# Optimization experiments

Measured on AMD Instinct MI355X. Metric: run time of the kernel, lower is better.

Reference implementation:

```python
import jax, jax.numpy as jnp
import numpy as np

EPS = 1e-12  # F.normalize eps

def _l2norm(x):
    n = jnp.linalg.norm(x, axis=-1, keepdims=True)
    return x / jnp.maximum(n, EPS)

def setup_inputs() -> dict:
    key = jax.random.key(0)
    ks = jax.random.split(key, 12)
    B, C, D, N, K = 64, 256, 128, 100000, 8
    inp = {
        "query_input": jax.random.normal(ks[0], (B, C), dtype=jnp.float32),
        "keys": jax.random.normal(ks[1], (N, D), dtype=jnp.float32),
        "values": jax.random.normal(ks[2], (N, D), dtype=jnp.float32),
        "importance": jax.random.uniform(ks[3], (N,), dtype=jnp.float32),
        # params (Linear weights stored torch-style: [out, in])
        "W_q": jax.random.normal(ks[4], (D, C), dtype=jnp.float32) / np.sqrt(C),
        "b_q": jax.random.normal(ks[5], (D,), dtype=jnp.float32) * 0.01,
        "w_attn": jax.random.normal(ks[6], (D,), dtype=jnp.float32) / np.sqrt(D),
        "b_attn": jax.random.normal(ks[7], (), dtype=jnp.float32) * 0.01,
        "W_comb": jax.random.normal(ks[8], (D, D), dtype=jnp.float32) / np.sqrt(D),
        "b_comb": jax.random.normal(ks[9], (D,), dtype=jnp.float32) * 0.01,
        "top_k": K,
    }
    return inp

def reference(query_input, keys, values, importance, W_q, b_q, w_attn, b_attn, W_comb, b_comb, top_k):
    # query projection: [B, D]
    q = query_input @ W_q.T + b_q
    # cosine similarity against every bank entry, importance-weighted: [B, N]
    sim = (_l2norm(q) @ _l2norm(keys).T) * importance[None, :]
    # top-k entries per batch row
    _, idx = jax.lax.top_k(sim, top_k)          # [B, K]
    retrieved = values[idx]                      # [B, K, D] gather
    # attention over the K retrieved memories
    scores = jax.nn.softmax(retrieved @ w_attn + b_attn, axis=-1)  # [B, K]
    memory_output = jnp.einsum("bk,bkd->bd", scores, retrieved)
    return memory_output @ W_comb.T + b_comb
```

## Files before the change

kernel.cpp:

```cpp
#include <hip/hip_runtime.h>

typedef __attribute__((ext_vector_type(8))) short short8;
typedef __attribute__((ext_vector_type(4))) float f32x4;

#define BB 64
#define CC 256
#define DD 128
#define NN 100000
#define KK 8

#define CHUNK 128
#define NBLK ((NN + CHUNK - 1) / CHUNK)
#define CPB (NBLK * KK)

__device__ __forceinline__ unsigned short f2bf(float x) {
    unsigned u = __float_as_uint(x);
    unsigned r = u + 0x7fffu + ((u >> 16) & 1u);
    return (unsigned short)(r >> 16);
}

__device__ __forceinline__ void split_bf(float x, unsigned short& h, unsigned short& l) {
    h = f2bf(x);
    float hf = __uint_as_float(((unsigned)h) << 16);
    l = f2bf(x - hf);
}

__device__ __forceinline__ void bfins8(float x, float l[8]) {
#pragma unroll
    for (int s = 0; s < 8; ++s) {
        float hi = fmaxf(l[s], x);
        x = fminf(l[s], x);
        l[s] = hi;
    }
}

__device__ __forceinline__ void bpins8(float v, int ix, float lv[8], int li[8]) {
#pragma unroll
    for (int s = 0; s < 8; ++s) {
        const bool gt = v > lv[s];
        const float nv = gt ? lv[s] : v;
        const int   ni = gt ? li[s] : ix;
        lv[s] = gt ? v : lv[s];
        li[s] = gt ? ix : li[s];
        v = nv; ix = ni;
    }
}

__global__ __launch_bounds__(128) void qproj_kernel(
    const float* __restrict__ query,
    const float* __restrict__ Wq,
    const float* __restrict__ bq,
    unsigned short* __restrict__ qAhi,
    unsigned short* __restrict__ qAlo)
{
    __shared__ float qrow[CC];
    const int tid = threadIdx.x;
    const int b = blockIdx.x;
    for (int i = tid; i < CC; i += 128) qrow[i] = query[b * CC + i];
    __syncthreads();
    float acc = bq[tid];
    const float4* wr = reinterpret_cast<const float4*>(Wq + (size_t)tid * CC);
#pragma unroll 8
    for (int c = 0; c < CC / 4; ++c) {
        float4 w = wr[c];
        acc = fmaf(w.x, qrow[c * 4 + 0], acc);
        acc = fmaf(w.y, qrow[c * 4 + 1], acc);
        acc = fmaf(w.z, qrow[c * 4 + 2], acc);
        acc = fmaf(w.w, qrow[c * 4 + 3], acc);
    }
    unsigned short h, l;
    split_bf(acc, h, l);
    const int d = tid;
    const int mt = b >> 4, n = b & 15;
    const int ks = d >> 5, quad = (d >> 3) & 3, j = d & 7;
    const size_t fi = ((size_t)(mt * 4 + ks) * 64 + quad * 16 + n) * 8 + j;
    qAhi[fi] = h;
    qAlo[fi] = l;
}

__global__ __launch_bounds__(256, 4) void simtopk_kernel(
    const unsigned short* __restrict__ qAhi,
    const unsigned short* __restrict__ qAlo,
    const float* __restrict__ keys,
    const float* __restrict__ imp,
    float* __restrict__ cand_v)
{
    __shared__ float sims[64 * 132];

    const int tid = threadIdx.x;
    const int w = tid >> 6, lane = tid & 63;
    const int p = w >> 1;
    const int h = w & 1;
    const int blk = blockIdx.x;
    const int key0 = blk * CHUNK;
    const int n = lane & 15, quad = lane >> 4;

    short8 Ah[2][4], Al[2][4];
    {
        const short8* GH = reinterpret_cast<const short8*>(qAhi);
        const short8* GL = reinterpret_cast<const short8*>(qAlo);
#pragma unroll
        for (int m2 = 0; m2 < 2; ++m2)
#pragma unroll
            for (int ks = 0; ks < 4; ++ks) {
                const int idx = ((p * 2 + m2) * 4 + ks) * 64 + lane;
                Ah[m2][ks] = GH[idx];
                Al[m2][ks] = GL[idx];
            }
    }

#pragma unroll
    for (int t = 0; t < 4; ++t) {
        const int jl = h * 64 + t * 16 + n;
        const int j = key0 + jl;
        const int jc = (j < NN) ? j : (NN - 1);
        const float* kb = keys + (size_t)jc * DD + quad * 8;

        float4 bv[8];
#pragma unroll
        for (int ks = 0; ks < 4; ++ks) {
            bv[2 * ks]     = *reinterpret_cast<const float4*>(kb + ks * 32);
            bv[2 * ks + 1] = *reinterpret_cast<const float4*>(kb + ks * 32 + 4);
        }

        f32x4 acc[2];
        acc[0] = (f32x4){0.f, 0.f, 0.f, 0.f};
        acc[1] = (f32x4){0.f, 0.f, 0.f, 0.f};
        float ss = 0.f;

#pragma unroll
        for (int ks = 0; ks < 4; ++ks) {
            const float f[8] = {bv[2*ks].x, bv[2*ks].y, bv[2*ks].z, bv[2*ks].w,
                                bv[2*ks+1].x, bv[2*ks+1].y, bv[2*ks+1].z, bv[2*ks+1].w};
            unsigned hw[4], lw[4];
#pragma unroll
            for (int e = 0; e < 4; ++e) {
                const float f0 = f[2 * e], f1 = f[2 * e + 1];
                const unsigned u0 = __float_as_uint(f0), u1 = __float_as_uint(f1);
                hw[e] = __builtin_amdgcn_perm(u1, u0, 0x07060302u);
                const float d0 = f0 - __uint_as_float(u0 & 0xffff0000u);
                const float d1 = f1 - __uint_as_float(u1 & 0xffff0000u);
                lw[e] = __builtin_amdgcn_perm(__float_as_uint(d1), __float_as_uint(d0), 0x07060302u);
                ss = fmaf(f0, f0, fmaf(f1, f1, ss));
            }
            uint4 hv = {hw[0], hw[1], hw[2], hw[3]};
            uint4 lv = {lw[0], lw[1], lw[2], lw[3]};
            short8 Bh = *reinterpret_cast<short8*>(&hv);
            short8 Bl = *reinterpret_cast<short8*>(&lv);
#pragma unroll
            for (int m2 = 0; m2 < 2; ++m2) {
                acc[m2] = __builtin_amdgcn_mfma_f32_16x16x32_bf16(Ah[m2][ks], Bh, acc[m2], 0, 0, 0);
                acc[m2] = __builtin_amdgcn_mfma_f32_16x16x32_bf16(Ah[m2][ks], Bl, acc[m2], 0, 0, 0);
                acc[m2] = __builtin_amdgcn_mfma_f32_16x16x32_bf16(Al[m2][ks], Bh, acc[m2], 0, 0, 0);
            }
        }

        ss += __shfl_xor(ss, 16);
        ss += __shfl_xor(ss, 32);
        const bool valid = (j < NN);
        float scale = 0.f;
        if (valid) scale = imp[j] / fmaxf(sqrtf(ss), 1e-12f);

#pragma unroll
        for (int m2 = 0; m2 < 2; ++m2)
#pragma unroll
            for (int r = 0; r < 4; ++r) {
                const int row = (p * 2 + m2) * 16 + quad * 4 + r;
                const float v = valid ? acc[m2][r] * scale : -1e30f;
                const unsigned packed = (__float_as_uint(v) & ~0x7Fu) | (unsigned)jl;
                sims[row * 132 + jl] = __uint_as_float(packed);
            }
    }
    __syncthreads();

    float v8[8];
    {
        const int row = tid >> 2, part = tid & 3;
#pragma unroll
        for (int s = 0; s < 8; ++s) v8[s] = -1e30f;
        const int base = row * 132 + part * 32;
        const int st = ((row & 15) + part * 8) & 31;
        for (int i = 0; i < 32; ++i) {
            const int ia = (i + st) & 31;
            bfins8(sims[base + ia], v8);
        }
    }
    __syncthreads();

    {
        const int row = tid >> 2, part = tid & 3;
        float4* dst = reinterpret_cast<float4*>(&sims[row * 132 + part * 8]);
        dst[0] = (float4){v8[0], v8[1], v8[2], v8[3]};
        dst[1] = (float4){v8[4], v8[5], v8[6], v8[7]};
    }
    __syncthreads();

    if (tid < 64) {
        const int row = tid;
        float m8[8];
#pragma unroll
        for (int s = 0; s < 8; ++s) m8[s] = -1e30f;
        const int st = (3 * row) & 31;
        for (int u = 0; u < 32; ++u)
            bfins8(sims[row * 132 + ((u + st) & 31)], m8);
        float4* out4 = reinterpret_cast<float4*>(cand_v + (size_t)row * CPB + (size_t)blk * KK);
        out4[0] = (float4){m8[0], m8[1], m8[2], m8[3]};
        out4[1] = (float4){m8[4], m8[5], m8[6], m8[7]};
    }
}

__global__ __launch_bounds__(256) void mergefinish_kernel(
    const float* __restrict__ cand_v,
    const float* __restrict__ values,
    const float* __restrict__ w_attn,
    const float* __restrict__ b_attn,
    const float* __restrict__ W_comb,
    const float* __restrict__ b_comb,
    float* __restrict__ out)
{
    __shared__ float lv[256 * 8];
    __shared__ int   li[256 * 8];
    __shared__ int   tk[KK];
    __shared__ float red[KK][DD];
    __shared__ float tvals[KK];
    __shared__ float mem[DD];

    const int tid = threadIdx.x;
    const int row = blockIdx.x;

    {
        float v8[8]; int i8[8];
#pragma unroll
        for (int s = 0; s < 8; ++s) { v8[s] = -1e30f; i8[s] = 0; }
        const float4* cv4 = reinterpret_cast<const float4*>(cand_v + (size_t)row * CPB);
        for (int c4 = tid; c4 < CPB / 4; c4 += 256) {
            const float4 v = cv4[c4];
            const int c = c4 * 4;
            bpins8(v.x, c + 0, v8, i8);
            bpins8(v.y, c + 1, v8, i8);
            bpins8(v.z, c + 2, v8, i8);
            bpins8(v.w, c + 3, v8, i8);
        }
#pragma unroll
        for (int s = 0; s < 8; ++s) { lv[tid * 8 + s] = v8[s]; li[tid * 8 + s] = i8[s]; }
    }
    __syncthreads();

    if (tid < 64) {
        float m8[8]; int mi8[8];
#pragma unroll
        for (int s = 0; s < 8; ++s) { m8[s] = -1e30f; mi8[s] = 0; }
        for (int k2 = 0; k2 < 4; ++k2)
#pragma unroll
            for (int s = 0; s < 8; ++s)
                bpins8(lv[(tid + 64 * k2) * 8 + s], li[(tid + 64 * k2) * 8 + s], m8, mi8);
        for (int rd = 0; rd < KK; ++rd) {
            float m = m8[0];
#pragma unroll
            for (int d = 1; d < 64; d <<= 1) m = fmaxf(m, __shfl_xor(m, d));
            const unsigned long long msk = __ballot(m8[0] == m);
            const int wl = (int)(__ffsll((long long)msk) - 1);
            const int wc = __shfl(mi8[0], wl);
            if (tid == 0)
                tk[rd] = (wc >> 3) * CHUNK + (int)(__float_as_uint(m) & 127u);
            if (tid == wl) {
#pragma unroll
                for (int s = 0; s < 7; ++s) { m8[s] = m8[s + 1]; mi8[s] = mi8[s + 1]; }
                m8[7] = -1e30f;
            }
        }
    }
    __syncthreads();

    float vk[KK];
    if (tid < 128) {
#pragma unroll
        for (int k = 0; k < KK; ++k)
            vk[k] = values[(size_t)tk[k] * DD + tid];
        const float wa = w_attn[tid];
#pragma unroll
        for (int k = 0; k < KK; ++k) red[k][tid] = vk[k] * wa;
    }
    __syncthreads();
    if (tid < KK) {
        float s = 0.f;
        for (int i = 0; i < DD; ++i) s += red[tid][i];
        tvals[tid] = s + b_attn[0];
    }
    __syncthreads();
    if (tid < 128) {
        float m = tvals[0];
#pragma unroll
        for (int k = 1; k < KK; ++k) m = fmaxf(m, tvals[k]);
        float e[KK]; float se = 0.f;
#pragma unroll
        for (int k = 0; k < KK; ++k) { e[k] = expf(tvals[k] - m); se += e[k]; }
        const float inv = 1.f / se;
        float md = 0.f;
#pragma unroll
        for (int k = 0; k < KK; ++k) md += (e[k] * inv) * vk[k];
        mem[tid] = md;
    }
    __syncthreads();
    if (tid < 128) {
        float acc = b_comb[tid];
        const float4* wrow = reinterpret_cast<const float4*>(W_comb + (size_t)tid * DD);
#pragma unroll 8
        for (int c = 0; c < DD / 4; ++c) {
            float4 wv = wrow[c];
            acc = fmaf(wv.x, mem[c * 4 + 0], acc);
            acc = fmaf(wv.y, mem[c * 4 + 1], acc);
            acc = fmaf(wv.z, mem[c * 4 + 2], acc);
            acc = fmaf(wv.w, mem[c * 4 + 3], acc);
        }
        out[row * DD + tid] = acc;
    }
}

extern "C" void kernel_launch(void* const* d_in, const int* in_sizes, int n_in,
                              void* d_out, int out_size, void* d_ws, size_t ws_size,
                              hipStream_t stream) {
    const float* query  = (const float*)d_in[0];
    const float* keys   = (const float*)d_in[1];
    const float* values = (const float*)d_in[2];
    const float* imp    = (const float*)d_in[3];
    const float* Wq     = (const float*)d_in[4];
    const float* bq     = (const float*)d_in[5];
    const float* wattn  = (const float*)d_in[6];
    const float* battn  = (const float*)d_in[7];
    const float* Wcomb  = (const float*)d_in[8];
    const float* bcomb  = (const float*)d_in[9];

    unsigned short* qAhi = (unsigned short*)d_ws;
    unsigned short* qAlo = qAhi + 8192;
    float* cand_v = (float*)(qAlo + 8192);

    qproj_kernel<<<BB, 128, 0, stream>>>(query, Wq, bq, qAhi, qAlo);
    simtopk_kernel<<<NBLK, 256, 0, stream>>>(qAhi, qAlo, keys, imp, cand_v);
    mergefinish_kernel<<<BB, 256, 0, stream>>>(cand_v, values, wattn, battn,
                                               Wcomb, bcomb, (float*)d_out);
}
```

Before: 163.1 us.

## Use bitonic merge for per-block top-8 and swizzle shared sims layout

Replaces the final 32-way insertion-sort merge with three bitonic merges of sorted 8-lists, cutting serial compare work done by the single 64-thread wave. The padded shared layout gives way to an XOR swizzle, which shrinks LDS, and the launch bound moves to 5 blocks per CU. Key loads are now issued inside the k-loop instead of all up front, lowering register pressure in exchange for less load-level parallelism.

Measured after the change: 172.8 us. 5.9% more time.

```diff
diff --git a/kernel.cpp b/kernel.cpp
--- a/kernel.cpp
+++ b/kernel.cpp
@@ -44,6 +44,19 @@
         li[s] = gt ? ix : li[s];
         v = nv; ix = ni;
     }
+}
+
+__device__ __forceinline__ void merge8(const float a[8], const float b[8], float o[8]) {
+    float m[8];
+#pragma unroll
+    for (int i = 0; i < 8; ++i) m[i] = fmaxf(a[i], b[7 - i]);
+#define CE(i, j) { float hi = fmaxf(m[i], m[j]); float lo = fminf(m[i], m[j]); m[i] = hi; m[j] = lo; }
+    CE(0, 4) CE(1, 5) CE(2, 6) CE(3, 7)
+    CE(0, 2) CE(1, 3) CE(4, 6) CE(5, 7)
+    CE(0, 1) CE(2, 3) CE(4, 5) CE(6, 7)
+#undef CE
+#pragma unroll
+    for (int i = 0; i < 8; ++i) o[i] = m[i];
 }
 
 __global__ __launch_bounds__(128) void qproj_kernel(
@@ -78,14 +91,14 @@
     qAlo[fi] = l;
 }
 
-__global__ __launch_bounds__(256, 4) void simtopk_kernel(
+__global__ __launch_bounds__(256, 5) void simtopk_kernel(
     const unsigned short* __restrict__ qAhi,
     const unsigned short* __restrict__ qAlo,
     const float* __restrict__ keys,
     const float* __restrict__ imp,
     float* __restrict__ cand_v)
 {
-    __shared__ float sims[64 * 132];
+    __shared__ float sims[64 * 128];
 
     const int tid = threadIdx.x;
     const int w = tid >> 6, lane = tid & 63;
@@ -116,13 +129,6 @@
         const int jc = (j < NN) ? j : (NN - 1);
         const float* kb = keys + (size_t)jc * DD + quad * 8;
 
-        float4 bv[8];
-#pragma unroll
-        for (int ks = 0; ks < 4; ++ks) {
-            bv[2 * ks]     = *reinterpret_cast<const float4*>(kb + ks * 32);
-            bv[2 * ks + 1] = *reinterpret_cast<const float4*>(kb + ks * 32 + 4);
-        }
-
         f32x4 acc[2];
         acc[0] = (f32x4){0.f, 0.f, 0.f, 0.f};
         acc[1] = (f32x4){0.f, 0.f, 0.f, 0.f};
@@ -130,8 +136,9 @@
 
 #pragma unroll
         for (int ks = 0; ks < 4; ++ks) {
-            const float f[8] = {bv[2*ks].x, bv[2*ks].y, bv[2*ks].z, bv[2*ks].w,
-                                bv[2*ks+1].x, bv[2*ks+1].y, bv[2*ks+1].z, bv[2*ks+1].w};
+            const float4 b0 = *reinterpret_cast<const float4*>(kb + ks * 32);
+            const float4 b1 = *reinterpret_cast<const float4*>(kb + ks * 32 + 4);
+            const float f[8] = {b0.x, b0.y, b0.z, b0.w, b1.x, b1.y, b1.z, b1.w};
             unsigned hw[4], lw[4];
 #pragma unroll
             for (int e = 0; e < 4; ++e) {
@@ -168,7 +175,7 @@
                 const int row = (p * 2 + m2) * 16 + quad * 4 + r;
                 const float v = valid ? acc[m2][r] * scale : -1e30f;
                 const unsigned packed = (__float_as_uint(v) & ~0x7Fu) | (unsigned)jl;
-                sims[row * 132 + jl] = __uint_as_float(packed);
+                sims[row * 128 + (jl ^ ((row & 4) << 2))] = __uint_as_float(packed);
             }
     }
     __syncthreads();
@@ -178,31 +185,38 @@
         const int row = tid >> 2, part = tid & 3;
 #pragma unroll
         for (int s = 0; s < 8; ++s) v8[s] = -1e30f;
-        const int base = row * 132 + part * 32;
-        const int st = ((row & 15) + part * 8) & 31;
-        for (int i = 0; i < 32; ++i) {
-            const int ia = (i + st) & 31;
-            bfins8(sims[base + ia], v8);
-        }
+        const float* rp = &sims[row * 128 + part * 32];
+        const int sc = (row & 15) ^ (part << 3);
+        for (int i = 0; i < 32; ++i)
+            bfins8(rp[(i ^ sc) & 31], v8);
     }
     __syncthreads();
 
     {
         const int row = tid >> 2, part = tid & 3;
-        float4* dst = reinterpret_cast<float4*>(&sims[row * 132 + part * 8]);
-        dst[0] = (float4){v8[0], v8[1], v8[2], v8[3]};
-        dst[1] = (float4){v8[4], v8[5], v8[6], v8[7]};
+        const int rot = (row & 7) * 4;
+#pragma unroll
+        for (int s = 0; s < 8; ++s)
+            sims[row * 128 + ((4 * s + part + rot) & 31)] = v8[s];
     }
     __syncthreads();
 
     if (tid < 64) {
         const int row = tid;
-        float m8[8];
-#pragma unroll
-        for (int s = 0; s < 8; ++s) m8[s] = -1e30f;
-        const int st = (3 * row) & 31;
-        for (int u = 0; u < 32; ++u)
-            bfins8(sims[row * 132 + ((u + st) & 31)], m8);
+        const int rot = (row & 7) * 4;
+        float l0[8], l1[8], l2[8], l3[8];
+#pragma unroll
+        for (int s = 0; s < 8; ++s) {
+            const float* rp = &sims[row * 128];
+            l0[s] = rp[(4 * s + 0 + rot) & 31];
+            l1[s] = rp[(4 * s + 1 + rot) & 31];
+            l2[s] = rp[(4 * s + 2 + rot) & 31];
+            l3[s] = rp[(4 * s + 3 + rot) & 31];
+        }
+        float m01[8], m23[8], m8[8];
+        merge8(l0, l1, m01);
+        merge8(l2, l3, m23);
+        merge8(m01, m23, m8);
         float4* out4 = reinterpret_cast<float4*>(cand_v + (size_t)row * CPB + (size_t)blk * KK);
         out4[0] = (float4){m8[0], m8[1], m8[2], m8[3]};
         out4[1] = (float4){m8[4], m8[5], m8[6], m8[7]};
```
